# Performance work log

Hardware: AMD Instinct MI355X
Metric: run time of the kernel (lower is better)

Reference implementation:

```python
import jax, jax.numpy as jnp
import numpy as np

EPS = 1e-6


def _make_coord_3d(D, H, W, dtype):
    # torch make_coord_3d(flatten=False).permute(3,0,1,2): channels stacked as (x, y, z)
    lz = jnp.linspace(-1.0, 1.0, D, dtype=dtype)
    ly = jnp.linspace(-1.0, 1.0, H, dtype=dtype)
    lx = jnp.linspace(-1.0, 1.0, W, dtype=dtype)
    cz, cy, cx = jnp.meshgrid(lz, ly, lx, indexing='ij')
    return jnp.stack([cx, cy, cz], axis=0)  # [3, D, H, W]


def _trilinear_border(vol, gd, gh, gw):
    # vol: [C, D, H, W]; gd/gh/gw: [Q] normalized coords for the D/H/W axes.
    # Matches torch grid_sample(mode='bilinear', align_corners=False, padding_mode='border').
    C, D, H, W = vol.shape
    z = (gd + 1.0) * (D * 0.5) - 0.5
    y = (gh + 1.0) * (H * 0.5) - 0.5
    x = (gw + 1.0) * (W * 0.5) - 0.5
    z0 = jnp.floor(z); y0 = jnp.floor(y); x0 = jnp.floor(x)
    wz = (z - z0)[None]; wy = (y - y0)[None]; wx = (x - x0)[None]  # [1, Q]
    z0i = jnp.clip(z0.astype(jnp.int32), 0, D - 1); z1i = jnp.clip(z0.astype(jnp.int32) + 1, 0, D - 1)
    y0i = jnp.clip(y0.astype(jnp.int32), 0, H - 1); y1i = jnp.clip(y0.astype(jnp.int32) + 1, 0, H - 1)
    x0i = jnp.clip(x0.astype(jnp.int32), 0, W - 1); x1i = jnp.clip(x0.astype(jnp.int32) + 1, 0, W - 1)
    g = lambda zi, yi, xi: vol[:, zi, yi, xi]  # gather -> [C, Q]
    return (g(z0i, y0i, x0i) * (1 - wz) * (1 - wy) * (1 - wx)
            + g(z0i, y0i, x1i) * (1 - wz) * (1 - wy) * wx
            + g(z0i, y1i, x0i) * (1 - wz) * wy * (1 - wx)
            + g(z0i, y1i, x1i) * (1 - wz) * wy * wx
            + g(z1i, y0i, x0i) * wz * (1 - wy) * (1 - wx)
            + g(z1i, y0i, x1i) * wz * (1 - wy) * wx
            + g(z1i, y1i, x0i) * wz * wy * (1 - wx)
            + g(z1i, y1i, x1i) * wz * wy * wx)


def _forward(inp, coord, cell, W0, b0, W1, b1, W2, b2, W3, b3):
    feat = inp  # identity encoder: inp is the latent feature grid
    B, C, D, H, W = feat.shape
    rx = 2.0 / D / 2.0; ry = 2.0 / H / 2.0; rz = 2.0 / W / 2.0
    sizes = jnp.array([D, H, W], dtype=feat.dtype)
    feat_coord = _make_coord_3d(D, H, W, feat.dtype)  # [3, D, H, W]
    sample_b = jax.vmap(_trilinear_border, in_axes=(0, 0, 0, 0))
    sample_c = jax.vmap(_trilinear_border, in_axes=(None, 0, 0, 0))

    rel_cell = cell * sizes  # [B, Q, 3]
    cell_vol = jnp.abs(cell[..., 0] * cell[..., 1] * cell[..., 2])
    scale_sq = jnp.clip(8.0 / (cell_vol + 1e-8), 1.0, 64.0)[..., None]  # [B, Q, 1]

    def mlp(x):
        h = jax.nn.relu(x @ W0 + b0)
        h = jax.nn.relu(h @ W1 + b1)
        h = jax.nn.relu(h @ W2 + b2)
        return h @ W3 + b3

    preds, areas = [], []
    for vx in (-1, 1):
        for vy in (-1, 1):
            for vz in (-1, 1):
                shift = jnp.array([vx * rx + EPS, vy * ry + EPS, vz * rz + EPS], dtype=coord.dtype)
                c = jnp.clip(coord + shift, -1.0 + 1e-6, 1.0 - 1e-6)
                gd, gh, gw = c[..., 0], c[..., 1], c[..., 2]
                q_feat = sample_b(feat, gd, gh, gw).transpose(0, 2, 1)        # [B, Q, C]
                q_coord = sample_c(feat_coord, gd, gh, gw).transpose(0, 2, 1)  # [B, Q, 3]
                rel_coord = (coord - q_coord) * sizes
                x = jnp.concatenate([q_feat, rel_coord, rel_cell, scale_sq], axis=-1)
                preds.append(mlp(x))  # [B, Q, 1]
                areas.append(jnp.abs(rel_coord[..., 0] * rel_coord[..., 1] * rel_coord[..., 2]) + 1e-9)
    tot_area = jnp.stack(areas).sum(axis=0)
    areas = areas[::-1]  # local-ensemble diagonal-swap of areas
    ret = sum(p * (a / tot_area)[..., None] for p, a in zip(preds, areas))
    return ret


def setup_inputs() -> dict:
    key = jax.random.key(0)
    ks = jax.random.split(key, 8)
    B, C, D, Q, HID = 1, 64, 32, 131072, 256
    in_dim = C + 3 + 3 + 1  # 71
    w = lambda k, shape, fan_in: jax.random.normal(k, shape, jnp.float32) * (1.0 / np.sqrt(fan_in))
    inp = jax.random.normal(ks[0], (B, C, D, D, D), jnp.float32)
    coord = jax.random.uniform(ks[1], (B, Q, 3), jnp.float32, -1.0, 1.0)
    cell = jnp.full((B, Q, 3), 2.0 / 64.0, jnp.float32)  # uniform cell size of a 64^3 query grid
    return {
        'inp': inp, 'coord': coord, 'cell': cell,
        'W0': w(ks[2], (in_dim, HID), in_dim), 'b0': jnp.zeros((HID,), jnp.float32),
        'W1': w(ks[3], (HID, HID), HID), 'b1': jnp.zeros((HID,), jnp.float32),
        'W2': w(ks[4], (HID, HID), HID), 'b2': jnp.zeros((HID,), jnp.float32),
        'W3': w(ks[5], (HID, 1), HID), 'b3': jnp.zeros((1,), jnp.float32),
    }


def reference(inp, coord, cell, W0, b0, W1, b1, W2, b2, W3, b3):
    return _forward(inp, coord, cell, W0, b0, W1, b1, W2, b2, W3, b3)
```

## Files before the change

kernel.cpp:

```cpp
#include <hip/hip_runtime.h>

typedef __attribute__((ext_vector_type(8))) short s16x8;
typedef __attribute__((ext_vector_type(4))) float f32x4;

__device__ __forceinline__ unsigned short f2bf(float x) {
  unsigned u = __float_as_uint(x);
  u = (u + 0x7fffu + ((u >> 16) & 1u)) >> 16;
  return (unsigned short)u;
}
__device__ __forceinline__ unsigned cvt_pk_bf16(float a, float b) {
  unsigned r;
  asm("v_cvt_pk_bf16_f32 %0, %1, %2" : "=v"(r) : "v"(a), "v"(b));
  return r;
}
__device__ __forceinline__ float bflo(unsigned v) { return __uint_as_float(v << 16); }
__device__ __forceinline__ float bfhi(unsigned v) { return __uint_as_float(v & 0xffff0000u); }

#define FEAT_OFF 0
#define W0F_OFF  2097152
#define W1F_OFF  (W0F_OFF + 24576)
#define W2F_OFF  (W1F_OFF + 65536)
#define W3P_OFF  (W2F_OFF + 65536)
#define WS_TOTAL (W3P_OFF + 512)

__device__ __forceinline__ int col_log(int kp) {
  return (kp & 0xC0) | ((kp & 3) << 4) | ((kp >> 2) & 15);
}

__global__ void liif_prep(const float* __restrict__ inp,
                          const float* __restrict__ W0,
                          const float* __restrict__ W1,
                          const float* __restrict__ W2,
                          const float* __restrict__ W3,
                          unsigned short* __restrict__ ws) {
  int tid = blockIdx.x * 256 + threadIdx.x;
  if (tid < 2097152) {
    int pos = tid >> 6, c = tid & 63;
    ws[FEAT_OFF + tid] = f2bf(inp[c * 32768 + pos]);
  } else if (tid < W1F_OFF) {
    int e = tid - W0F_OFF;
    int j = e & 7, L = (e >> 3) & 63, nt = (e >> 9) & 15, c = e >> 13;
    int k = c * 32 + (L >> 4) * 8 + j, n = nt * 16 + (L & 15);
    ws[tid] = (k < 71) ? f2bf(W0[k * 256 + n]) : (unsigned short)0;
  } else if (tid < W2F_OFF) {
    int e = tid - W1F_OFF;
    int j = e & 7, L = (e >> 3) & 63, nt = (e >> 9) & 15, c = e >> 13;
    int kp = c * 32 + (L >> 4) * 8 + j, n = nt * 16 + (L & 15);
    ws[tid] = f2bf(W1[col_log(kp) * 256 + n]);
  } else if (tid < W3P_OFF) {
    int e = tid - W2F_OFF;
    int j = e & 7, L = (e >> 3) & 63, nt = (e >> 9) & 15, c = e >> 13;
    int kp = c * 32 + (L >> 4) * 8 + j, n = nt * 16 + (L & 15);
    ws[tid] = f2bf(W2[col_log(kp) * 256 + n]);
  } else if (tid < W3P_OFF + 256) {
    int e = tid - W3P_OFF;
    float* w3p = (float*)(ws + W3P_OFF);
    w3p[e] = W3[col_log(e)];
  }
}

template<int KC>
__device__ __forceinline__ void run_layer(const unsigned short* __restrict__ Wf,
                                          const float* __restrict__ bias,
                                          const unsigned short* A, int astride,
                                          unsigned short* H,
                                          int wave, int quad, int l16, int lane) {
  f32x4 acc[4][4];
#pragma unroll
  for (int i = 0; i < 4; ++i)
#pragma unroll
    for (int j = 0; j < 4; ++j) acc[i][j] = (f32x4){0.f, 0.f, 0.f, 0.f};

#pragma unroll
  for (int c = 0; c < KC; ++c) {
    s16x8 a[4];
#pragma unroll
    for (int rt = 0; rt < 4; ++rt)
      a[rt] = *(const s16x8*)(A + (rt * 16 + l16) * astride + c * 32 + quad * 8);
#pragma unroll
    for (int ntl = 0; ntl < 4; ++ntl) {
      int nt = wave * 4 + ntl;
      s16x8 b = *(const s16x8*)(Wf + (((c * 16 + nt) * 64 + lane) << 3));
#pragma unroll
      for (int rt = 0; rt < 4; ++rt)
        acc[rt][ntl] = __builtin_amdgcn_mfma_f32_16x16x32_bf16(a[rt], b, acc[rt][ntl], 0, 0, 0);
    }
  }
  __syncthreads();

  float bv[4];
#pragma unroll
  for (int ntl = 0; ntl < 4; ++ntl) bv[ntl] = bias[(wave * 4 + ntl) * 16 + l16];

  const int cbase = wave * 64 + l16 * 4;
#pragma unroll
  for (int rt = 0; rt < 4; ++rt) {
#pragma unroll
    for (int i = 0; i < 4; ++i) {
      float v0 = fmaxf(acc[rt][0][i] + bv[0], 0.0f);
      float v1 = fmaxf(acc[rt][1][i] + bv[1], 0.0f);
      float v2 = fmaxf(acc[rt][2][i] + bv[2], 0.0f);
      float v3 = fmaxf(acc[rt][3][i] + bv[3], 0.0f);
      int r = rt * 16 + quad * 4 + i;
      uint2 pw = make_uint2(cvt_pk_bf16(v0, v1), cvt_pk_bf16(v2, v3));
      *(uint2*)(H + r * 264 + cbase) = pw;
    }
  }
  __syncthreads();
}

__global__ __launch_bounds__(256, 4)
void liif_main(const float* __restrict__ coord,
               const float* __restrict__ cell,
               const float* __restrict__ b0,
               const float* __restrict__ b1,
               const float* __restrict__ b2,
               const float* __restrict__ b3,
               const unsigned short* __restrict__ ws,
               float* __restrict__ out) {
  __shared__ __align__(16) unsigned short sm_h[64 * 264];
  __shared__ float sm_area[64];
  __shared__ float sm_pred[64];
  unsigned short* sm_x = sm_h;

  const unsigned short* feat = ws + FEAT_OFF;
  const int tid = threadIdx.x;
  const int lane = tid & 63;
  const int wave = tid >> 6;
  const int quad = lane >> 4;
  const int l16 = lane & 15;

  {
    const int row = tid >> 2, p = tid & 3;
    const int ql = row >> 3, s = row & 7;
    const int q = blockIdx.x * 8 + ql;
    const float c0r = coord[q * 3 + 0], c1r = coord[q * 3 + 1], c2r = coord[q * 3 + 2];
    const float R = 0.03125f;
    const float sh0 = ((s & 4) ? R : -R) + 1e-6f;
    const float sh1 = ((s & 2) ? R : -R) + 1e-6f;
    const float sh2 = ((s & 1) ? R : -R) + 1e-6f;
    const float LO = -1.0f + 1e-6f, HI = 1.0f - 1e-6f;
    float c0 = fminf(fmaxf(c0r + sh0, LO), HI);
    float c1 = fminf(fmaxf(c1r + sh1, LO), HI);
    float c2 = fminf(fmaxf(c2r + sh2, LO), HI);
    float z = (c0 + 1.0f) * 16.0f - 0.5f;
    float y = (c1 + 1.0f) * 16.0f - 0.5f;
    float x = (c2 + 1.0f) * 16.0f - 0.5f;
    float zf = floorf(z), yf = floorf(y), xf = floorf(x);
    float wz = z - zf, wy = y - yf, wx = x - xf;
    int z0 = min(max((int)zf, 0), 31), z1 = min(max((int)zf + 1, 0), 31);
    int y0 = min(max((int)yf, 0), 31), y1 = min(max((int)yf + 1, 0), 31);
    int x0 = min(max((int)xf, 0), 31), x1 = min(max((int)xf + 1, 0), 31);
    float wz0 = 1.0f - wz, wy0 = 1.0f - wy, wx0 = 1.0f - wx;

    float w[8] = { wz0 * wy0 * wx0, wz0 * wy0 * wx, wz0 * wy * wx0, wz0 * wy * wx,
                   wz  * wy0 * wx0, wz  * wy0 * wx, wz  * wy * wx0, wz  * wy * wx };
    int idx[8] = { (z0 * 32 + y0) * 32 + x0, (z0 * 32 + y0) * 32 + x1,
                   (z0 * 32 + y1) * 32 + x0, (z0 * 32 + y1) * 32 + x1,
                   (z1 * 32 + y0) * 32 + x0, (z1 * 32 + y0) * 32 + x1,
                   (z1 * 32 + y1) * 32 + x0, (z1 * 32 + y1) * 32 + x1 };

    float acc[16];
#pragma unroll
    for (int i = 0; i < 16; ++i) acc[i] = 0.0f;
#pragma unroll
    for (int corner = 0; corner < 8; ++corner) {
      const uint4* cp = (const uint4*)(feat + idx[corner] * 64 + p * 16);
      uint4 v0 = cp[0], v1 = cp[1];
      float wc = w[corner];
      unsigned vv[8] = { v0.x, v0.y, v0.z, v0.w, v1.x, v1.y, v1.z, v1.w };
#pragma unroll
      for (int d = 0; d < 8; ++d) {
        acc[2 * d]     += wc * bflo(vv[d]);
        acc[2 * d + 1] += wc * bfhi(vv[d]);
      }
    }
    unsigned pw[8];
#pragma unroll
    for (int d = 0; d < 8; ++d)
      pw[d] = cvt_pk_bf16(acc[2 * d], acc[2 * d + 1]);
    uint4* dst = (uint4*)(&sm_x[row * 104 + p * 16]);
    dst[0] = make_uint4(pw[0], pw[1], pw[2], pw[3]);
    dst[1] = make_uint4(pw[4], pw[5], pw[6], pw[7]);

    if (p == 0) {
      const float step = 2.0f / 31.0f;
      float qc0 = wx0 * (-1.0f + step * x0) + wx * (-1.0f + step * x1);
      float qc1 = wy0 * (-1.0f + step * y0) + wy * (-1.0f + step * y1);
      float qc2 = wz0 * (-1.0f + step * z0) + wz * (-1.0f + step * z1);
      float rel0 = (c0r - qc0) * 32.0f;
      float rel1 = (c1r - qc1) * 32.0f;
      float rel2 = (c2r - qc2) * 32.0f;
      sm_area[row] = fabsf(rel0 * rel1 * rel2) + 1e-9f;
      float cl0 = cell[q * 3 + 0], cl1 = cell[q * 3 + 1], cl2 = cell[q * 3 + 2];
      float ssq = fminf(fmaxf(8.0f / (fabsf(cl0 * cl1 * cl2) + 1e-8f), 1.0f), 64.0f);
      unsigned tw0 = cvt_pk_bf16(rel0, rel1);
      unsigned tw1 = cvt_pk_bf16(rel2, cl0 * 32.0f);
      unsigned tw2 = cvt_pk_bf16(cl1 * 32.0f, cl2 * 32.0f);
      unsigned tw3 = cvt_pk_bf16(ssq, 0.0f);
      uint4* d2 = (uint4*)(&sm_x[row * 104 + 64]);
      d2[0] = make_uint4(tw0, tw1, tw2, tw3);
      d2[1] = make_uint4(0, 0, 0, 0);
      d2[2] = make_uint4(0, 0, 0, 0);
      d2[3] = make_uint4(0, 0, 0, 0);
    }
  }
  __syncthreads();

  run_layer<3>(ws + W0F_OFF, b0, sm_x, 104, sm_h, wave, quad, l16, lane);
  run_layer<8>(ws + W1F_OFF, b1, sm_h, 264, sm_h, wave, quad, l16, lane);
  run_layer<8>(ws + W2F_OFF, b2, sm_h, 264, sm_h, wave, quad, l16, lane);

  {
    const int row = tid >> 2, p = tid & 3;
    const unsigned short* hp = sm_h + row * 264 + p * 64;
    const float* W3p = (const float*)(ws + W3P_OFF);
    float sum = 0.0f;
#pragma unroll
    for (int kk = 0; kk < 8; ++kk) {
      const uint4 v = *(const uint4*)(hp + kk * 8);
      const float4 wa = *(const float4*)(W3p + p * 64 + kk * 8);
      const float4 wb = *(const float4*)(W3p + p * 64 + kk * 8 + 4);
      sum += wa.x * bflo(v.x) + wa.y * bfhi(v.x);
      sum += wa.z * bflo(v.y) + wa.w * bfhi(v.y);
      sum += wb.x * bflo(v.z) + wb.y * bfhi(v.z);
      sum += wb.z * bflo(v.w) + wb.w * bfhi(v.w);
    }
    sum += __shfl_xor(sum, 1);
    sum += __shfl_xor(sum, 2);
    if (p == 0) sm_pred[row] = sum + b3[0];
  }
  __syncthreads();

  if (tid < 8) {
    const int ql = tid;
    float tot = 0.0f, ret = 0.0f;
#pragma unroll
    for (int s = 0; s < 8; ++s) tot += sm_area[ql * 8 + s];
#pragma unroll
    for (int s = 0; s < 8; ++s) ret += sm_pred[ql * 8 + s] * sm_area[ql * 8 + (7 - s)];
    out[blockIdx.x * 8 + ql] = ret / tot;
  }
}

extern "C" void kernel_launch(void* const* d_in, const int* in_sizes, int n_in,
                              void* d_out, int out_size, void* d_ws, size_t ws_size,
                              hipStream_t stream) {
  const float* inp   = (const float*)d_in[0];
  const float* coord = (const float*)d_in[1];
  const float* cell  = (const float*)d_in[2];
  const float* W0    = (const float*)d_in[3];
  const float* b0    = (const float*)d_in[4];
  const float* W1    = (const float*)d_in[5];
  const float* b1    = (const float*)d_in[6];
  const float* W2    = (const float*)d_in[7];
  const float* b2    = (const float*)d_in[8];
  const float* W3    = (const float*)d_in[9];
  const float* b3    = (const float*)d_in[10];
  unsigned short* ws = (unsigned short*)d_ws;
  float* out = (float*)d_out;

  const int Q = in_sizes[1] / 3;
  hipLaunchKernelGGL(liif_prep, dim3((WS_TOTAL + 255) / 256), dim3(256), 0, stream,
                     inp, W0, W1, W2, W3, ws);
  hipLaunchKernelGGL(liif_main, dim3(Q / 8), dim3(256), 0, stream,
                     coord, cell, b0, b1, b2, b3, ws, out);
}
```

Measured before the change: 461.9 us.

## Prefetch next layer's first weight chunk and use LDS-only barriers

Each layer now loads the first weight K-chunk of the next layer into registers before the epilogue barrier. This hides global-load latency at the start of each MLP layer. The __syncthreads calls become an lgkmcnt-only wait plus s_barrier, so outstanding global prefetches are not drained at each barrier. The bias load is hoisted ahead of the MFMA loop and s_setprio raises wave priority during the MFMA loop. Holding the prefetched values adds register pressure under launch_bounds(256,4).

```diff
diff --git a/kernel.cpp b/kernel.cpp
--- a/kernel.cpp
+++ b/kernel.cpp
@@ -15,6 +15,12 @@
 }
 __device__ __forceinline__ float bflo(unsigned v) { return __uint_as_float(v << 16); }
 __device__ __forceinline__ float bfhi(unsigned v) { return __uint_as_float(v & 0xffff0000u); }
+
+__device__ __forceinline__ void lgkm_barrier() {
+  asm volatile("s_waitcnt lgkmcnt(0)" ::: "memory");
+  __builtin_amdgcn_s_barrier();
+  asm volatile("" ::: "memory");
+}
 
 #define FEAT_OFF 0
 #define W0F_OFF  2097152
@@ -59,18 +65,25 @@
   }
 }
 
-template<int KC>
+template<int KC, bool PRE>
 __device__ __forceinline__ void run_layer(const unsigned short* __restrict__ Wf,
                                           const float* __restrict__ bias,
                                           const unsigned short* A, int astride,
                                           unsigned short* H,
+                                          const unsigned short* __restrict__ Wnext,
+                                          s16x8 (&nb)[4],
                                           int wave, int quad, int l16, int lane) {
+  float bv[4];
+#pragma unroll
+  for (int ntl = 0; ntl < 4; ++ntl) bv[ntl] = bias[(wave * 4 + ntl) * 16 + l16];
+
   f32x4 acc[4][4];
 #pragma unroll
   for (int i = 0; i < 4; ++i)
 #pragma unroll
     for (int j = 0; j < 4; ++j) acc[i][j] = (f32x4){0.f, 0.f, 0.f, 0.f};
 
+  __builtin_amdgcn_s_setprio(1);
 #pragma unroll
   for (int c = 0; c < KC; ++c) {
     s16x8 a[4];
@@ -80,17 +93,22 @@
 #pragma unroll
     for (int ntl = 0; ntl < 4; ++ntl) {
       int nt = wave * 4 + ntl;
-      s16x8 b = *(const s16x8*)(Wf + (((c * 16 + nt) * 64 + lane) << 3));
+      s16x8 b = (c == 0) ? nb[ntl]
+                         : *(const s16x8*)(Wf + (((c * 16 + nt) * 64 + lane) << 3));
 #pragma unroll
       for (int rt = 0; rt < 4; ++rt)
         acc[rt][ntl] = __builtin_amdgcn_mfma_f32_16x16x32_bf16(a[rt], b, acc[rt][ntl], 0, 0, 0);
     }
   }
-  __syncthreads();
-
-  float bv[4];
-#pragma unroll
-  for (int ntl = 0; ntl < 4; ++ntl) bv[ntl] = bias[(wave * 4 + ntl) * 16 + l16];
+  __builtin_amdgcn_s_setprio(0);
+
+  if constexpr (PRE) {
+#pragma unroll
+    for (int ntl = 0; ntl < 4; ++ntl)
+      nb[ntl] = *(const s16x8*)(Wnext + (((wave * 4 + ntl) * 64 + lane) << 3));
+  }
+
+  lgkm_barrier();
 
   const int cbase = wave * 64 + l16 * 4;
 #pragma unroll
@@ -106,7 +124,7 @@
       *(uint2*)(H + r * 264 + cbase) = pw;
     }
   }
-  __syncthreads();
+  lgkm_barrier();
 }
 
 __global__ __launch_bounds__(256, 4)
@@ -129,6 +147,11 @@
   const int wave = tid >> 6;
   const int quad = lane >> 4;
   const int l16 = lane & 15;
+
+  s16x8 nb[4];
+#pragma unroll
+  for (int ntl = 0; ntl < 4; ++ntl)
+    nb[ntl] = *(const s16x8*)(ws + W0F_OFF + (((wave * 4 + ntl) * 64 + lane) << 3));
 
   {
     const int row = tid >> 2, p = tid & 3;
@@ -205,11 +228,11 @@
       d2[3] = make_uint4(0, 0, 0, 0);
     }
   }
-  __syncthreads();
-
-  run_layer<3>(ws + W0F_OFF, b0, sm_x, 104, sm_h, wave, quad, l16, lane);
-  run_layer<8>(ws + W1F_OFF, b1, sm_h, 264, sm_h, wave, quad, l16, lane);
-  run_layer<8>(ws + W2F_OFF, b2, sm_h, 264, sm_h, wave, quad, l16, lane);
+  lgkm_barrier();
+
+  run_layer<3, true >(ws + W0F_OFF, b0, sm_x, 104, sm_h, ws + W1F_OFF, nb, wave, quad, l16, lane);
+  run_layer<8, true >(ws + W1F_OFF, b1, sm_h, 264, sm_h, ws + W2F_OFF, nb, wave, quad, l16, lane);
+  run_layer<8, false>(ws + W2F_OFF, b2, sm_h, 264, sm_h, nullptr,      nb, wave, quad, l16, lane);
 
   {
     const int row = tid >> 2, p = tid & 3;
@@ -230,7 +253,7 @@
     sum += __shfl_xor(sum, 2);
     if (p == 0) sm_pred[row] = sum + b3[0];
   }
-  __syncthreads();
+  lgkm_barrier();
 
   if (tid < 8) {
     const int ql = tid;
```

After: 439.8 us. 1.05x faster.
